# Performance work log

Hardware: AMD Instinct MI355X
Metric: run time of the kernel (lower is better)

## Reference

```python
import jax, jax.numpy as jnp
import numpy as np
import math

D_MODEL = 128
N_HEAD = 8
D_K = D_MODEL // N_HEAD
NEG_INF = -1e30


def setup_inputs() -> dict:
    key = jax.random.key(0)
    ks = jax.random.split(key, 8)
    B, N, D = 4, 2048, D_MODEL
    s = 1.0 / math.sqrt(D)
    x = jax.random.normal(ks[0], (B, D, N), dtype=jnp.float32)
    mask = jnp.ones((B, N), dtype=jnp.float32)
    Wq = jax.random.normal(ks[1], (D, D), dtype=jnp.float32) * s
    Wk = jax.random.normal(ks[2], (D, D), dtype=jnp.float32) * s
    Wv = jax.random.normal(ks[3], (D, D), dtype=jnp.float32) * s
    Wfc = jax.random.normal(ks[4], (D, D), dtype=jnp.float32) * s
    z = jnp.zeros((D,), dtype=jnp.float32)
    return {"x": x, "mask": mask, "Wq": Wq, "bq": z, "Wk": Wk, "bk": z,
            "Wv": Wv, "bv": z, "Wfc": Wfc, "bfc": z}


def reference(x, mask, Wq, bq, Wk, bk, Wv, bv, Wfc, bfc):
    # x: [B, D, N], mask: [B, N]
    B, D, N = x.shape
    xt = jnp.swapaxes(x, 1, 2)  # [B, N, D]
    q = (xt @ Wq.T + bq).reshape(B, N, N_HEAD, D_K)
    k = (xt @ Wk.T + bk).reshape(B, N, N_HEAD, D_K)
    v = (xt @ Wv.T + bv).reshape(B, N, N_HEAD, D_K)
    # scores: [B, H, Nq, Nk]; NOTE: original scales by sqrt(d_model), not sqrt(d_k)
    scores = jnp.einsum('bnhd,bmhd->bhnm', q, k) / jnp.sqrt(jnp.float32(D))
    # multiplicative mask_logits over the key dimension
    m = mask[:, None, None, :]  # [B, 1, 1, Nk]
    scores = scores * m + (1.0 - m) * NEG_INF
    atten = jax.nn.softmax(scores, axis=-1)  # dropout is identity (p=0 / eval)
    out = jnp.einsum('bhnm,bmhd->bnhd', atten, v).reshape(B, N, D)
    out = out @ Wfc.T + bfc
    return jnp.swapaxes(out, 1, 2)  # [B, D, N]
```

## Files before the change

### kernel.cpp

```cpp
#include <hip/hip_runtime.h>
#include <stdint.h>

#define BSZ  4
#define NSEQ 2048
#define DM   128
#define NH   8
#define DK   16
#define LOG2E 1.4426950408889634f
#define SCALE_QL 0.1275156338341935f
#define W_SCALE 3.814697265625e-6f

typedef __bf16          bf16x8v __attribute__((ext_vector_type(8)));
typedef float           f32x4   __attribute__((ext_vector_type(4)));
typedef float           f32x16  __attribute__((ext_vector_type(16)));
typedef unsigned short  u16x8   __attribute__((ext_vector_type(8)));
typedef unsigned short  u16x4   __attribute__((ext_vector_type(4)));
typedef unsigned int    u32x2   __attribute__((ext_vector_type(2)));
typedef unsigned int    u32x4   __attribute__((ext_vector_type(4)));

__device__ __forceinline__ unsigned short f2bf(float f) {
    unsigned u = __float_as_uint(f);
    u = (u + 0x7fffu + ((u >> 16) & 1u)) >> 16;
    return (unsigned short)u;
}

__device__ __forceinline__ unsigned int pack2bf(float a, float b) {
#if __has_builtin(__builtin_amdgcn_cvt_pk_bf16_f32)
    typedef __bf16 bf16x2 __attribute__((ext_vector_type(2)));
    bf16x2 v = __builtin_amdgcn_cvt_pk_bf16_f32(a, b);
    return __builtin_bit_cast(unsigned int, v);
#else
    return (unsigned)f2bf(a) | ((unsigned)f2bf(b) << 16);
#endif
}

__device__ __forceinline__ float exp2_(float x) {
#if __has_builtin(__builtin_amdgcn_exp2f)
    return __builtin_amdgcn_exp2f(x);
#else
    return exp2f(x);
#endif
}

__device__ __forceinline__ f32x4 mfma16(u16x8 a, u16x8 b, f32x4 c) {
    return __builtin_amdgcn_mfma_f32_16x16x32_bf16(
        __builtin_bit_cast(bf16x8v, a), __builtin_bit_cast(bf16x8v, b), c, 0, 0, 0);
}
__device__ __forceinline__ f32x16 mfma32(u16x8 a, u16x8 b, f32x16 c) {
    return __builtin_amdgcn_mfma_f32_32x32x16_bf16(
        __builtin_bit_cast(bf16x8v, a), __builtin_bit_cast(bf16x8v, b), c, 0, 0, 0);
}

__device__ __forceinline__ void xpair(unsigned lo, unsigned hi_, int bpi, int isHi,
                                      unsigned& wA, unsigned& wB) {
    const unsigned send = isHi ? lo : hi_;
    const unsigned recv =
        (unsigned)__builtin_amdgcn_ds_bpermute(bpi, (int)send);
    wA = isHi ? recv : lo;
    wB = isHi ? hi_ : recv;
}

__global__ __launch_bounds__(256) void k_prep(
    const float* __restrict__ Wq, const float* __restrict__ Wk,
    const float* __restrict__ Wv, const float* __restrict__ Wfc,
    const float* __restrict__ mask,
    unsigned short* __restrict__ WqB, unsigned short* __restrict__ WkB,
    unsigned short* __restrict__ WvB, unsigned short* __restrict__ WfcB,
    unsigned short* __restrict__ VW2)
{
    const int gt = blockIdx.x * 256 + threadIdx.x;
    if (gt < DM * DM) {
        WqB[gt]  = f2bf(Wq[gt] * SCALE_QL);
        WkB[gt]  = f2bf(Wk[gt]);
        WvB[gt]  = f2bf(Wv[gt]);
        WfcB[gt] = f2bf(Wfc[gt]);
    } else if (gt < DM * DM + BSZ * NSEQ) {
        const int i  = gt - DM * DM;
        const int kv = i & (NSEQ - 1);
        const int bb = i >> 11;
        const unsigned short w16 = f2bf(mask[i] * W_SCALE);
        unsigned short* dst = VW2 +
            (((size_t)(bb * NH) * 128 + (kv >> 4)) << 9) +
            (16 + ((kv >> 3) & 1) * 32) * 8 + (kv & 7);
#pragma unroll
        for (int hh = 0; hh < NH; ++hh)
            dst[(size_t)hh * 128 * 512] = w16;
    }
}

__global__ __launch_bounds__(768) void k_qkv(
    const float* __restrict__ x,
    const unsigned short* __restrict__ WqB, const float* __restrict__ bq,
    const unsigned short* __restrict__ WkB, const float* __restrict__ bk,
    const unsigned short* __restrict__ WvB, const float* __restrict__ bv,
    const float* __restrict__ mask,
    unsigned short* __restrict__ Q, unsigned short* __restrict__ Kb,
    unsigned short* __restrict__ VW2)
{
    __shared__ __align__(16) float xs[DM * 36];
    const int tid = threadIdx.x;

    const int b  = blockIdx.x >> 6;
    const int n0 = (blockIdx.x & 63) << 5;

#pragma unroll
    for (int i = tid; i < 1024; i += 768) {
        const int d = i >> 3, c4 = (i & 7) << 2;
        *reinterpret_cast<f32x4*>(&xs[d * 36 + c4]) =
            *reinterpret_cast<const f32x4*>(x + (size_t)(b * DM + d) * NSEQ + n0 + c4);
    }
    __syncthreads();

    const int lane = tid & 63;
    const int wv   = tid >> 6;
    const int mat  = wv >> 2;
    const int nt   = (wv >> 1) & 1;
    const int th   = wv & 1;
    const int c    = lane & 15;
    const int quad = lane >> 4;
    const int col  = n0 + nt * 16 + c;

    u16x8 xf[4];
#pragma unroll
    for (int kk = 0; kk < 4; ++kk) {
        float f[8];
#pragma unroll
        for (int j = 0; j < 8; ++j)
            f[j] = xs[(kk * 32 + quad * 8 + j) * 36 + nt * 16 + c];
        u32x4 u = {pack2bf(f[0], f[1]), pack2bf(f[2], f[3]),
                   pack2bf(f[4], f[5]), pack2bf(f[6], f[7])};
        xf[kk] = __builtin_bit_cast(u16x8, u);
    }

    const unsigned short* W = (mat == 0) ? WqB : (mat == 1) ? WkB : WvB;
    const float* bias = (mat == 0) ? bq : (mat == 1) ? bk : bv;
    const float  sc   = (mat == 0) ? SCALE_QL : 1.0f;
    const float  vwsc = (mat == 2) ? mask[b * NSEQ + col] * W_SCALE : 0.f;
    const int    g    = col >> 4;
    const int    roff = ((col >> 3) & 1) * 32;
    const int    j7   = col & 7;

#pragma unroll
    for (int tt = 0; tt < 4; ++tt) {
        const int t = th * 4 + tt;
        f32x4 acc = {0.f, 0.f, 0.f, 0.f};
#pragma unroll
        for (int kk = 0; kk < 4; ++kk)
            acc = mfma16(*reinterpret_cast<const u16x8*>(
                             W + (t * 16 + c) * DM + kk * 32 + quad * 8),
                         xf[kk], acc);
        if (mat == 2) {
            unsigned short* vwp = VW2 +
                (((size_t)((b * NH + t) * 128 + g)) << 9) + j7;
#pragma unroll
            for (int r = 0; r < 4; ++r)
                vwp[(quad * 4 + r + roff) * 8] =
                    f2bf((acc[r] + bias[t * 16 + quad * 4 + r]) * vwsc);
        } else {
            u16x4 pk;
#pragma unroll
            for (int r = 0; r < 4; ++r)
                pk[r] = f2bf(acc[r] + bias[t * 16 + quad * 4 + r] * sc);
            *reinterpret_cast<u16x4*>(
                (mat == 0 ? Q : Kb) + ((size_t)(b * NH + t) * NSEQ + col) * DK +
                quad * 4) = pk;
        }
    }
}

__global__ __launch_bounds__(256, 4) void k_attn(
    const unsigned short* __restrict__ Q,
    const unsigned short* __restrict__ Kb,
    const unsigned short* __restrict__ VW2,
    unsigned short* __restrict__ AO)
{
    __shared__ __align__(16) float smem[128 + 4 * 32 * 20];
    const int tid  = threadIdx.x;
    const int lane = tid & 63;
    const int w    = tid >> 6;
    const int q32  = lane & 31;
    const int hi   = lane >> 5;
    const int bpi  = (lane ^ 32) << 2;

    const int bid = ((int)blockIdx.x & 7) * 256 + ((int)blockIdx.x >> 3);
    const int b  = bid >> 9;
    const int h  = (bid >> 6) & 7;
    const int n0 = (bid & 63) << 5;
    const int bh = b * NH + h;

    const u16x8 uq = *reinterpret_cast<const u16x8*>(
        Q + ((size_t)bh * NSEQ + n0 + q32) * DK + 8 * hi);

    const unsigned short* Kp = Kb + (size_t)bh * NSEQ * DK + 8 * hi;
    const unsigned short* Ap = VW2 + (((size_t)bh * 128) << 9) + lane * 8;

    f32x16 acc = {};
    const f32x16 z16 = {};
    const int kvb = w * (NSEQ / 4);

    u16x8 nk0 = *reinterpret_cast<const u16x8*>(Kp + (size_t)(kvb + q32) * DK);
    u16x8 nk1 = *reinterpret_cast<const u16x8*>(Kp + (size_t)(kvb + 32 + q32) * DK);

#pragma unroll 1
    for (int it = 0; it < 8; ++it) {
        const int kv0 = kvb + it * 64;
        const int g0  = kv0 >> 4;
        const u16x8 va0 = *reinterpret_cast<const u16x8*>(Ap + ((size_t)(g0    ) << 9));
        const u16x8 va1 = *reinterpret_cast<const u16x8*>(Ap + ((size_t)(g0 + 1) << 9));
        const u16x8 va2 = *reinterpret_cast<const u16x8*>(Ap + ((size_t)(g0 + 2) << 9));
        const u16x8 va3 = *reinterpret_cast<const u16x8*>(Ap + ((size_t)(g0 + 3) << 9));

        u16x8 bf1, bf2;
        {
            __builtin_amdgcn_s_setprio(1);
            f32x16 S = mfma32(nk0, uq, z16);
            __builtin_amdgcn_s_setprio(0);
            if (it < 7)
                nk0 = *reinterpret_cast<const u16x8*>(
                    Kp + (size_t)(kv0 + 64 + q32) * DK);
#pragma unroll
            for (int i = 0; i < 16; ++i) S[i] = exp2_(S[i]);
            const unsigned a0 = pack2bf(S[0],  S[1]),  a1 = pack2bf(S[2],  S[3]);
            const unsigned b0 = pack2bf(S[4],  S[5]),  b1 = pack2bf(S[6],  S[7]);
            const unsigned c0 = pack2bf(S[8],  S[9]),  c1 = pack2bf(S[10], S[11]);
            const unsigned d0 = pack2bf(S[12], S[13]), d1 = pack2bf(S[14], S[15]);
            unsigned w0, w1, w2, w3, y0, y1, y2, y3;
            xpair(a0, b0, bpi, hi, w0, w2);
            xpair(a1, b1, bpi, hi, w1, w3);
            xpair(c0, d0, bpi, hi, y0, y2);
            xpair(c1, d1, bpi, hi, y1, y3);
            const u32x4 f1 = {w0, w1, w2, w3};
            const u32x4 f2 = {y0, y1, y2, y3};
            bf1 = __builtin_bit_cast(u16x8, f1);
            bf2 = __builtin_bit_cast(u16x8, f2);
        }
        __builtin_amdgcn_s_setprio(1);
        acc = mfma32(va0, bf1, acc);
        acc = mfma32(va1, bf2, acc);
        __builtin_amdgcn_s_setprio(0);

        u16x8 bf3, bf4;
        {
            __builtin_amdgcn_s_setprio(1);
            f32x16 S = mfma32(nk1, uq, z16);
            __builtin_amdgcn_s_setprio(0);
            if (it < 7)
                nk1 = *reinterpret_cast<const u16x8*>(
                    Kp + (size_t)(kv0 + 96 + q32) * DK);
#pragma unroll
            for (int i = 0; i < 16; ++i) S[i] = exp2_(S[i]);
            const unsigned a0 = pack2bf(S[0],  S[1]),  a1 = pack2bf(S[2],  S[3]);
            const unsigned b0 = pack2bf(S[4],  S[5]),  b1 = pack2bf(S[6],  S[7]);
            const unsigned c0 = pack2bf(S[8],  S[9]),  c1 = pack2bf(S[10], S[11]);
            const unsigned d0 = pack2bf(S[12], S[13]), d1 = pack2bf(S[14], S[15]);
            unsigned w0, w1, w2, w3, y0, y1, y2, y3;
            xpair(a0, b0, bpi, hi, w0, w2);
            xpair(a1, b1, bpi, hi, w1, w3);
            xpair(c0, d0, bpi, hi, y0, y2);
            xpair(c1, d1, bpi, hi, y1, y3);
            const u32x4 f3 = {w0, w1, w2, w3};
            const u32x4 f4 = {y0, y1, y2, y3};
            bf3 = __builtin_bit_cast(u16x8, f3);
            bf4 = __builtin_bit_cast(u16x8, f4);
        }
        __builtin_amdgcn_s_setprio(1);
        acc = mfma32(va2, bf3, acc);
        acc = mfma32(va3, bf4, acc);
        __builtin_amdgcn_s_setprio(0);
    }

    float* Lsm = smem;
    float* Osm = smem + 128;
    float* Orow = Osm + w * 640 + q32 * 20;
    *reinterpret_cast<f32x4*>(Orow + (hi ? 4 : 0)) =
        f32x4{acc[0], acc[1], acc[2], acc[3]};
    *reinterpret_cast<f32x4*>(Orow + (hi ? 12 : 8)) =
        f32x4{acc[4], acc[5], acc[6], acc[7]};
    if (!hi) Lsm[w * 32 + q32] = acc[8];
    __syncthreads();

    const int q   = tid >> 3;
    const int dk2 = (tid & 7) * 2;
    const float l = Lsm[q] + Lsm[32 + q] + Lsm[64 + q] + Lsm[96 + q];
    const float* Oq = Osm + q * 20 + dk2;
    const float v0 = Oq[0] + Oq[640] + Oq[1280] + Oq[1920];
    const float v1 = Oq[1] + Oq[641] + Oq[1281] + Oq[1921];
    const float inv = 1.0f / l;
    *reinterpret_cast<unsigned int*>(
        AO + ((size_t)(b * NSEQ) + n0 + q) * DM + h * DK + dk2) =
        pack2bf(v0 * inv, v1 * inv);
}

__global__ __launch_bounds__(256) void k_fc(
    const unsigned short* __restrict__ AO,
    const unsigned short* __restrict__ WfcB, const float* __restrict__ bfc,
    float* __restrict__ out)
{
    const int lane = threadIdx.x & 63;
    const int w    = threadIdx.x >> 6;
    const int c    = lane & 15;
    const int quad = lane >> 4;
    const int b    = blockIdx.x >> 8;
    const int n0   = ((blockIdx.x >> 1) & 127) << 4;
    const int t    = (blockIdx.x & 1) * 4 + w;

    u16x8 af[4];
#pragma unroll
    for (int kk = 0; kk < 4; ++kk)
        af[kk] = *reinterpret_cast<const u16x8*>(
            AO + ((size_t)(b * NSEQ) + n0 + c) * DM + kk * 32 + quad * 8);

    f32x4 acc = {0.f, 0.f, 0.f, 0.f};
#pragma unroll
    for (int kk = 0; kk < 4; ++kk)
        acc = mfma16(*reinterpret_cast<const u16x8*>(
                         WfcB + (t * 16 + c) * DM + kk * 32 + quad * 8),
                     af[kk], acc);
#pragma unroll
    for (int r = 0; r < 4; ++r)
        out[(size_t)(b * DM + t * 16 + quad * 4 + r) * NSEQ + n0 + c] =
            acc[r] + bfc[t * 16 + quad * 4 + r];
}

extern "C" void kernel_launch(void* const* d_in, const int* in_sizes, int n_in,
                              void* d_out, int out_size, void* d_ws, size_t ws_size,
                              hipStream_t stream)
{
    const float* x    = (const float*)d_in[0];
    const float* mask = (const float*)d_in[1];
    const float* Wq   = (const float*)d_in[2];
    const float* bq   = (const float*)d_in[3];
    const float* Wk   = (const float*)d_in[4];
    const float* bk   = (const float*)d_in[5];
    const float* Wv   = (const float*)d_in[6];
    const float* bv   = (const float*)d_in[7];
    const float* Wfc  = (const float*)d_in[8];
    const float* bfc  = (const float*)d_in[9];
    float* out = (float*)d_out;

    const size_t QKV_ELEMS = (size_t)BSZ * NH * NSEQ * DK;
    unsigned short* Q    = (unsigned short*)d_ws;
    unsigned short* Kb   = Q + QKV_ELEMS;
    unsigned short* AO   = Kb + QKV_ELEMS;
    unsigned short* WfcB = AO + QKV_ELEMS;
    unsigned short* VW2  = WfcB + DM * DM;
    unsigned short* WqB  = VW2 + (size_t)BSZ * NH * 128 * 512;
    unsigned short* WkB  = WqB + DM * DM;
    unsigned short* WvB  = WkB + DM * DM;

    k_prep<<<96, 256, 0, stream>>>(Wq, Wk, Wv, Wfc, mask,
                                   WqB, WkB, WvB, WfcB, VW2);
    k_qkv<<<256, 768, 0, stream>>>(x, WqB, bq, WkB, bk, WvB, bv, mask,
                                   Q, Kb, VW2);
    k_attn<<<2048, 256, 0, stream>>>(Q, Kb, VW2, AO);
    k_fc<<<1024, 256, 0, stream>>>(AO, WfcB, bfc, out);
}
```

Baseline: 120.4 us.

## Process two query tiles per attention block to reuse K and V fragments

Each k_attn block now handles 64 queries as two 32-query tiles instead of one. The K and V fragment loads from global memory are shared between both tiles, halving K/V traffic per query, and the grid shrinks from 2048 to 1024 blocks. The cost is higher register pressure from two accumulators and two score tiles, a doubled shared-memory reduction buffer, and fewer blocks in flight, which could reduce occupancy or hurt latency hiding.

```diff
diff --git a/kernel.cpp b/kernel.cpp
--- a/kernel.cpp
+++ b/kernel.cpp
@@ -58,6 +58,23 @@
         (unsigned)__builtin_amdgcn_ds_bpermute(bpi, (int)send);
     wA = isHi ? recv : lo;
     wB = isHi ? hi_ : recv;
+}
+
+__device__ __forceinline__ void build_bfrags(const f32x16& S, int bpi, int hi,
+                                             u16x8& bfe, u16x8& bfo) {
+    const unsigned a0 = pack2bf(S[0],  S[1]),  a1 = pack2bf(S[2],  S[3]);
+    const unsigned b0 = pack2bf(S[4],  S[5]),  b1 = pack2bf(S[6],  S[7]);
+    const unsigned c0 = pack2bf(S[8],  S[9]),  c1 = pack2bf(S[10], S[11]);
+    const unsigned d0 = pack2bf(S[12], S[13]), d1 = pack2bf(S[14], S[15]);
+    unsigned w0, w1, w2, w3, y0, y1, y2, y3;
+    xpair(a0, b0, bpi, hi, w0, w2);
+    xpair(a1, b1, bpi, hi, w1, w3);
+    xpair(c0, d0, bpi, hi, y0, y2);
+    xpair(c1, d1, bpi, hi, y1, y3);
+    const u32x4 f1 = {w0, w1, w2, w3};
+    const u32x4 f2 = {y0, y1, y2, y3};
+    bfe = __builtin_bit_cast(u16x8, f1);
+    bfo = __builtin_bit_cast(u16x8, f2);
 }
 
 __global__ __launch_bounds__(256) void k_prep(
@@ -174,7 +191,7 @@
     const unsigned short* __restrict__ VW2,
     unsigned short* __restrict__ AO)
 {
-    __shared__ __align__(16) float smem[128 + 4 * 32 * 20];
+    __shared__ __align__(16) float smem[256 + 2 * 4 * 32 * 20];
     const int tid  = threadIdx.x;
     const int lane = tid & 63;
     const int w    = tid >> 6;
@@ -182,19 +199,22 @@
     const int hi   = lane >> 5;
     const int bpi  = (lane ^ 32) << 2;
 
-    const int bid = ((int)blockIdx.x & 7) * 256 + ((int)blockIdx.x >> 3);
-    const int b  = bid >> 9;
-    const int h  = (bid >> 6) & 7;
-    const int n0 = (bid & 63) << 5;
+    const int bid = ((int)blockIdx.x & 7) * 128 + ((int)blockIdx.x >> 3);
+    const int b  = bid >> 8;
+    const int h  = (bid >> 5) & 7;
+    const int n0 = (bid & 31) << 6;
     const int bh = b * NH + h;
 
-    const u16x8 uq = *reinterpret_cast<const u16x8*>(
+    const u16x8 uqA = *reinterpret_cast<const u16x8*>(
         Q + ((size_t)bh * NSEQ + n0 + q32) * DK + 8 * hi);
+    const u16x8 uqB = *reinterpret_cast<const u16x8*>(
+        Q + ((size_t)bh * NSEQ + n0 + 32 + q32) * DK + 8 * hi);
 
     const unsigned short* Kp = Kb + (size_t)bh * NSEQ * DK + 8 * hi;
     const unsigned short* Ap = VW2 + (((size_t)bh * 128) << 9) + lane * 8;
 
-    f32x16 acc = {};
+    f32x16 accA = {};
+    f32x16 accB = {};
     const f32x16 z16 = {};
     const int kvb = w * (NSEQ / 4);
 
@@ -210,85 +230,85 @@
         const u16x8 va2 = *reinterpret_cast<const u16x8*>(Ap + ((size_t)(g0 + 2) << 9));
         const u16x8 va3 = *reinterpret_cast<const u16x8*>(Ap + ((size_t)(g0 + 3) << 9));
 
-        u16x8 bf1, bf2;
         {
             __builtin_amdgcn_s_setprio(1);
-            f32x16 S = mfma32(nk0, uq, z16);
+            f32x16 SA = mfma32(nk0, uqA, z16);
+            f32x16 SB = mfma32(nk0, uqB, z16);
             __builtin_amdgcn_s_setprio(0);
             if (it < 7)
                 nk0 = *reinterpret_cast<const u16x8*>(
                     Kp + (size_t)(kv0 + 64 + q32) * DK);
 #pragma unroll
-            for (int i = 0; i < 16; ++i) S[i] = exp2_(S[i]);
-            const unsigned a0 = pack2bf(S[0],  S[1]),  a1 = pack2bf(S[2],  S[3]);
-            const unsigned b0 = pack2bf(S[4],  S[5]),  b1 = pack2bf(S[6],  S[7]);
-            const unsigned c0 = pack2bf(S[8],  S[9]),  c1 = pack2bf(S[10], S[11]);
-            const unsigned d0 = pack2bf(S[12], S[13]), d1 = pack2bf(S[14], S[15]);
-            unsigned w0, w1, w2, w3, y0, y1, y2, y3;
-            xpair(a0, b0, bpi, hi, w0, w2);
-            xpair(a1, b1, bpi, hi, w1, w3);
-            xpair(c0, d0, bpi, hi, y0, y2);
-            xpair(c1, d1, bpi, hi, y1, y3);
-            const u32x4 f1 = {w0, w1, w2, w3};
-            const u32x4 f2 = {y0, y1, y2, y3};
-            bf1 = __builtin_bit_cast(u16x8, f1);
-            bf2 = __builtin_bit_cast(u16x8, f2);
+            for (int i = 0; i < 16; ++i) SA[i] = exp2_(SA[i]);
+#pragma unroll
+            for (int i = 0; i < 16; ++i) SB[i] = exp2_(SB[i]);
+            u16x8 bfA1, bfA2, bfB1, bfB2;
+            build_bfrags(SA, bpi, hi, bfA1, bfA2);
+            build_bfrags(SB, bpi, hi, bfB1, bfB2);
+            __builtin_amdgcn_s_setprio(1);
+            accA = mfma32(va0, bfA1, accA);
+            accB = mfma32(va0, bfB1, accB);
+            accA = mfma32(va1, bfA2, accA);
+            accB = mfma32(va1, bfB2, accB);
+            __builtin_amdgcn_s_setprio(0);
         }
-        __builtin_amdgcn_s_setprio(1);
-        acc = mfma32(va0, bf1, acc);
-        acc = mfma32(va1, bf2, acc);
-        __builtin_amdgcn_s_setprio(0);
-
-        u16x8 bf3, bf4;
+
         {
             __builtin_amdgcn_s_setprio(1);
-            f32x16 S = mfma32(nk1, uq, z16);
+            f32x16 SA = mfma32(nk1, uqA, z16);
+            f32x16 SB = mfma32(nk1, uqB, z16);
             __builtin_amdgcn_s_setprio(0);
             if (it < 7)
                 nk1 = *reinterpret_cast<const u16x8*>(
                     Kp + (size_t)(kv0 + 96 + q32) * DK);
 #pragma unroll
-            for (int i = 0; i < 16; ++i) S[i] = exp2_(S[i]);
-            const unsigned a0 = pack2bf(S[0],  S[1]),  a1 = pack2bf(S[2],  S[3]);
-            const unsigned b0 = pack2bf(S[4],  S[5]),  b1 = pack2bf(S[6],  S[7]);
-            const unsigned c0 = pack2bf(S[8],  S[9]),  c1 = pack2bf(S[10], S[11]);
-            const unsigned d0 = pack2bf(S[12], S[13]), d1 = pack2bf(S[14], S[15]);
-            unsigned w0, w1, w2, w3, y0, y1, y2, y3;
-            xpair(a0, b0, bpi, hi, w0, w2);
-            xpair(a1, b1, bpi, hi, w1, w3);
-            xpair(c0, d0, bpi, hi, y0, y2);
-            xpair(c1, d1, bpi, hi, y1, y3);
-            const u32x4 f3 = {w0, w1, w2, w3};
-            const u32x4 f4 = {y0, y1, y2, y3};
-            bf3 = __builtin_bit_cast(u16x8, f3);
-            bf4 = __builtin_bit_cast(u16x8, f4);
+            for (int i = 0; i < 16; ++i) SA[i] = exp2_(SA[i]);
+#pragma unroll
+            for (int i = 0; i < 16; ++i) SB[i] = exp2_(SB[i]);
+            u16x8 bfA1, bfA2, bfB1, bfB2;
+            build_bfrags(SA, bpi, hi, bfA1, bfA2);
+            build_bfrags(SB, bpi, hi, bfB1, bfB2);
+            __builtin_amdgcn_s_setprio(1);
+            accA = mfma32(va2, bfA1, accA);
+            accB = mfma32(va2, bfB1, accB);
+            accA = mfma32(va3, bfA2, accA);
+            accB = mfma32(va3, bfB2, accB);
+            __builtin_amdgcn_s_setprio(0);
         }
-        __builtin_amdgcn_s_setprio(1);
-        acc = mfma32(va2, bf3, acc);
-        acc = mfma32(va3, bf4, acc);
-        __builtin_amdgcn_s_setprio(0);
     }
 
     float* Lsm = smem;
-    float* Osm = smem + 128;
-    float* Orow = Osm + w * 640 + q32 * 20;
-    *reinterpret_cast<f32x4*>(Orow + (hi ? 4 : 0)) =
-        f32x4{acc[0], acc[1], acc[2], acc[3]};
-    *reinterpret_cast<f32x4*>(Orow + (hi ? 12 : 8)) =
-        f32x4{acc[4], acc[5], acc[6], acc[7]};
-    if (!hi) Lsm[w * 32 + q32] = acc[8];
+    float* Osm = smem + 256;
+    {
+        float* Orow = Osm + w * 640 + q32 * 20;
+        *reinterpret_cast<f32x4*>(Orow + (hi ? 4 : 0)) =
+            f32x4{accA[0], accA[1], accA[2], accA[3]};
+        *reinterpret_cast<f32x4*>(Orow + (hi ? 12 : 8)) =
+            f32x4{accA[4], accA[5], accA[6], accA[7]};
+        if (!hi) Lsm[w * 32 + q32] = accA[8];
+        float* Orow2 = Orow + 2560;
+        *reinterpret_cast<f32x4*>(Orow2 + (hi ? 4 : 0)) =
+            f32x4{accB[0], accB[1], accB[2], accB[3]};
+        *reinterpret_cast<f32x4*>(Orow2 + (hi ? 12 : 8)) =
+            f32x4{accB[4], accB[5], accB[6], accB[7]};
+        if (!hi) Lsm[128 + w * 32 + q32] = accB[8];
+    }
     __syncthreads();
 
     const int q   = tid >> 3;
     const int dk2 = (tid & 7) * 2;
-    const float l = Lsm[q] + Lsm[32 + q] + Lsm[64 + q] + Lsm[96 + q];
-    const float* Oq = Osm + q * 20 + dk2;
-    const float v0 = Oq[0] + Oq[640] + Oq[1280] + Oq[1920];
-    const float v1 = Oq[1] + Oq[641] + Oq[1281] + Oq[1921];
-    const float inv = 1.0f / l;
-    *reinterpret_cast<unsigned int*>(
-        AO + ((size_t)(b * NSEQ) + n0 + q) * DM + h * DK + dk2) =
-        pack2bf(v0 * inv, v1 * inv);
+#pragma unroll
+    for (int t2 = 0; t2 < 2; ++t2) {
+        const float* Lt = Lsm + t2 * 128;
+        const float l = Lt[q] + Lt[32 + q] + Lt[64 + q] + Lt[96 + q];
+        const float* Oq = Osm + t2 * 2560 + q * 20 + dk2;
+        const float v0 = Oq[0] + Oq[640] + Oq[1280] + Oq[1920];
+        const float v1 = Oq[1] + Oq[641] + Oq[1281] + Oq[1921];
+        const float inv = 1.0f / l;
+        *reinterpret_cast<unsigned int*>(
+            AO + ((size_t)(b * NSEQ) + n0 + t2 * 32 + q) * DM + h * DK + dk2) =
+            pack2bf(v0 * inv, v1 * inv);
+    }
 }
 
 __global__ __launch_bounds__(256) void k_fc(
@@ -352,6 +372,6 @@
                                    WqB, WkB, WvB, WfcB, VW2);
     k_qkv<<<256, 768, 0, stream>>>(x, WqB, bq, WkB, bk, WvB, bv, mask,
                                    Q, Kb, VW2);
-    k_attn<<<2048, 256, 0, stream>>>(Q, Kb, VW2, AO);
+    k_attn<<<1024, 256, 0, stream>>>(Q, Kb, VW2, AO);
     k_fc<<<1024, 256, 0, stream>>>(AO, WfcB, bfc, out);
 }
```

Result: no change. 118.3 us (-1.8%).
